# Performance work log

Measured on AMD Instinct MI355X. Metric: run time of the kernel, lower is better.

Reference implementation:

```python
import jax, jax.numpy as jnp
import numpy as np

T, B, I, H, NQ = 256, 256, 256, 512, 4

def setup_inputs() -> dict:
    key = jax.random.key(0)
    ks = jax.random.split(key, 16)
    d = {"inputs": jax.random.normal(ks[0], (T, B, I), dtype=jnp.float32)}
    idx = 1
    for n in ["f", "i", "g", "o"]:
        d[f"W{n}_l"] = jax.random.normal(ks[idx], (NQ, I + H), dtype=jnp.float32) * 0.02; idx += 1
        d[f"b{n}_l"] = jnp.zeros((NQ,), jnp.float32)
        d[f"W{n}_p"] = jax.random.normal(ks[idx], (H, 1), dtype=jnp.float32) * 0.5; idx += 1
        d[f"b{n}_p"] = jnp.zeros((H,), jnp.float32)
        d[f"W{n}_r"] = jax.random.normal(ks[idx], (H, H), dtype=jnp.float32) * 0.02; idx += 1
    return d

def reference(inputs, Wf_l, bf_l, Wf_p, bf_p, Wf_r,
              Wi_l, bi_l, Wi_p, bi_p, Wi_r,
              Wg_l, bg_l, Wg_p, bg_p, Wg_r,
              Wo_l, bo_l, Wo_p, bo_p, Wo_r):
    # Quantum circuit: RX(theta_i) on each wire, CNOT chain, <Z_0>. Only wire-0's
    # rotation affects Z_0 (CNOT(0,1) has wire 0 as control and commutes with Z_0),
    # so expval = cos(theta_0). theta = Linear(combined), take component 0.
    def gate(comb, hx, Wl, bl, Wp, bp, Wr, act):
        q = jnp.cos(comb @ Wl[0] + bl[0])[:, None]          # (B,1) = <Z_0>
        return act(q @ Wp.T + bp) + hx @ Wr.T               # proj + classical residual

    def step(carry, x):
        hx, cx = carry
        comb = jnp.concatenate([x, hx], axis=1)             # (B, I+H)
        f = gate(comb, hx, Wf_l, bf_l, Wf_p, bf_p, Wf_r, jax.nn.sigmoid)
        i = gate(comb, hx, Wi_l, bi_l, Wi_p, bi_p, Wi_r, jax.nn.sigmoid)
        g = gate(comb, hx, Wg_l, bg_l, Wg_p, bg_p, Wg_r, jnp.tanh)
        o = gate(comb, hx, Wo_l, bo_l, Wo_p, bo_p, Wo_r, jax.nn.sigmoid)
        cx = f * cx + i * g
        hx = o * jnp.tanh(cx)
        return (hx, cx), hx

    b = inputs.shape[1]
    h0 = jnp.zeros((b, H), inputs.dtype)
    (hx, cx), ys = jax.lax.scan(step, (h0, h0), inputs)
    return ys, hx, cx
```

## Files before the change

kernel.cpp:

```cpp
#include <hip/hip_runtime.h>
#include <hip/hip_cooperative_groups.h>
#include <math.h>

namespace cg = cooperative_groups;

#define T_ 256
#define B_ 256
#define I_ 256
#define H_ 512
#define NB 8
#define NH 32
#define BG 32
#define NTH 512

typedef __attribute__((ext_vector_type(8))) short short8;
typedef __attribute__((ext_vector_type(4))) float f32x4;
typedef __attribute__((ext_vector_type(4))) unsigned int uint4v;

__device__ __forceinline__ float sig_(float v){ return 1.0f/(1.0f+__expf(-v)); }
__device__ __forceinline__ short f2bf(float f){
  unsigned u = __float_as_uint(f);
  unsigned r = (u + 0x7fffu + ((u>>16)&1u)) >> 16;
  return (short)r;
}

__global__ __launch_bounds__(NTH)
void qlstm_kernel(
    const float* __restrict__ x,
    const float* __restrict__ Wf_l, const float* __restrict__ bf_l,
    const float* __restrict__ Wf_p, const float* __restrict__ bf_p,
    const float* __restrict__ Wf_r,
    const float* __restrict__ Wi_l, const float* __restrict__ bi_l,
    const float* __restrict__ Wi_p, const float* __restrict__ bi_p,
    const float* __restrict__ Wi_r,
    const float* __restrict__ Wg_l, const float* __restrict__ bg_l,
    const float* __restrict__ Wg_p, const float* __restrict__ bg_p,
    const float* __restrict__ Wg_r,
    const float* __restrict__ Wo_l, const float* __restrict__ bo_l,
    const float* __restrict__ Wo_p, const float* __restrict__ bo_p,
    const float* __restrict__ Wo_r,
    float* __restrict__ out,
    char* __restrict__ wsb)
{
  __shared__ char  hxT[32*1024];
  __shared__ float gacc[4*32*17];
  __shared__ float qd[4*32];
  __shared__ unsigned short hxe[32*16];

  float*          sx    = (float*)wsb;
  unsigned short* hxg   = (unsigned short*)(wsb + (1u<<20));
  unsigned*       flags = (unsigned*)(wsb + (1u<<20) + (256u<<10));

  const int tid  = threadIdx.x;
  const int wgid = blockIdx.x;
  const int bgp  = wgid & 7;
  const int nh   = wgid >> 3;
  const int wave = tid >> 6;
  const int l    = tid & 63;
  const int l15  = l & 15;
  const int q4   = l >> 4;
  const int m    = wave & 3;
  const int n    = wave >> 2;
  const bool hasq = (m == 0);

  for (int idx = tid; idx < 8*4*BG; idx += NTH) {
    int g   = idx >> 8;
    int rem = idx & 255;
    int tt  = rem >> 5;
    int b   = rem & 31;
    int t   = nh*8 + tt;
    int bglob = bgp*BG + b;
    const float* wl = (g==0)?Wf_l:(g==1)?Wi_l:(g==2)?Wg_l:Wo_l;
    const float* bl = (g==0)?bf_l:(g==1)?bi_l:(g==2)?bg_l:bo_l;
    const float* xr = x + ((size_t)t*B_ + bglob)*I_;
    float a = 0.f;
    #pragma unroll 8
    for (int i2 = 0; i2 < I_; i2 += 4) {
      float4 v = *(const float4*)(xr + i2);
      a += v.x*wl[i2] + v.y*wl[i2+1] + v.z*wl[i2+2] + v.w*wl[i2+3];
    }
    sx[((size_t)t*4 + g)*B_ + bglob] = a + bl[0];
  }
  if (tid < T_)
    __hip_atomic_store(&flags[((size_t)tid*8 + bgp)*32 + nh], 0u,
                       __ATOMIC_RELAXED, __HIP_MEMORY_SCOPE_SYSTEM);

  short8 afrag[16];
  short8 afragq[16];
  {
    const float* wr = (m==0)?Wf_r:(m==1)?Wi_r:(m==2)?Wg_r:Wo_r;
    const int h = nh*16 + l15;
    #pragma unroll
    for (int kk = 0; kk < 16; ++kk) {
      const float* src = wr + (size_t)h*H_ + kk*32 + q4*8;
      short8 pk;
      #pragma unroll
      for (int j = 0; j < 8; ++j) pk[j] = f2bf(src[j]);
      afrag[kk] = pk;
    }
    if (hasq) {
      #pragma unroll
      for (int kk = 0; kk < 16; ++kk) {
        short8 pk;
        if (l15 < 4) {
          const float* ql = (l15==0)?Wf_l:(l15==1)?Wi_l:(l15==2)?Wg_l:Wo_l;
          const float* src = ql + I_ + kk*32 + q4*8;
          #pragma unroll
          for (int j = 0; j < 8; ++j) pk[j] = f2bf(src[j]);
        } else {
          #pragma unroll
          for (int j = 0; j < 8; ++j) pk[j] = 0;
        }
        afragq[kk] = pk;
      }
    }
  }

  const int hl = tid & 15;
  const int eb = tid >> 4;
  const int h_ep = nh*16 + hl;
  const int bglob_ep = bgp*BG + eb;
  const float wfp = Wf_p[h_ep], bfp = bf_p[h_ep];
  const float wip = Wi_p[h_ep], bip = bi_p[h_ep];
  const float wgp = Wg_p[h_ep], bgp_ = bg_p[h_ep];
  const float wop = Wo_p[h_ep], bop = bo_p[h_ep];
  float cxr = 0.f;

  cg::grid_group grid = cg::this_grid();
  grid.sync();

  const int bb   = n*16 + l15;
  const int brow = bb * 1024;
  const int bsw  = (bb & 7) << 4;
  const int bq16 = q4 * 16;

  for (int t = 0; t < T_; ++t) {
    if (t == 0) {
      #pragma unroll
      for (int i = 0; i < 4; ++i)
        *(f32x4*)(hxT + ((wave*4+i)*1024 + 16*l)) = (f32x4){0.f,0.f,0.f,0.f};
    } else {
      uint4v v0, v1, v2, v3;
      unsigned long long base =
        (unsigned long long)((const char*)hxg + (((size_t)(bgp*BG + wave*4)) << 10) + 16*l);
      asm volatile("global_load_dwordx4 %0, %1, off sc0 sc1"             : "=v"(v0) : "v"(base) : "memory");
      asm volatile("global_load_dwordx4 %0, %1, off offset:1024 sc0 sc1" : "=v"(v1) : "v"(base) : "memory");
      asm volatile("global_load_dwordx4 %0, %1, off offset:2048 sc0 sc1" : "=v"(v2) : "v"(base) : "memory");
      asm volatile("global_load_dwordx4 %0, %1, off offset:3072 sc0 sc1" : "=v"(v3) : "v"(base) : "memory");
      asm volatile("s_waitcnt vmcnt(0)" ::: "memory");
      const int r0w = wave*4;
      *(uint4v*)(hxT + ((r0w  )*1024 + ((16*l) ^ (((r0w  )&7)<<4)))) = v0;
      *(uint4v*)(hxT + ((r0w+1)*1024 + ((16*l) ^ (((r0w+1)&7)<<4)))) = v1;
      *(uint4v*)(hxT + ((r0w+2)*1024 + ((16*l) ^ (((r0w+2)&7)<<4)))) = v2;
      *(uint4v*)(hxT + ((r0w+3)*1024 + ((16*l) ^ (((r0w+3)&7)<<4)))) = v3;
    }
    __syncthreads();

    f32x4 acc  = {0.f,0.f,0.f,0.f};
    f32x4 accq = {0.f,0.f,0.f,0.f};
    #pragma unroll
    for (int kk = 0; kk < 16; ++kk) {
      short8 bf = *(const short8*)(hxT + brow + ((kk*64 + bq16) ^ bsw));
      acc = __builtin_amdgcn_mfma_f32_16x16x32_bf16(afrag[kk], bf, acc, 0, 0, 0);
      if (hasq)
        accq = __builtin_amdgcn_mfma_f32_16x16x32_bf16(afragq[kk], bf, accq, 0, 0, 0);
    }
    {
      const int cb = n*16 + l15;
      const int r0 = q4*4;
      #pragma unroll
      for (int r = 0; r < 4; ++r)
        gacc[(m*32 + cb)*17 + r0 + r] = acc[r];
      if (hasq && q4 == 0) {
        #pragma unroll
        for (int r = 0; r < 4; ++r)
          qd[r*32 + cb] = accq[r];
      }
    }
    __syncthreads();

    float hnew;
    {
      float q0 = cosf(sx[((size_t)t*4+0)*B_ + bglob_ep] + qd[0*32+eb]);
      float q1 = cosf(sx[((size_t)t*4+1)*B_ + bglob_ep] + qd[1*32+eb]);
      float q2 = cosf(sx[((size_t)t*4+2)*B_ + bglob_ep] + qd[2*32+eb]);
      float q3 = cosf(sx[((size_t)t*4+3)*B_ + bglob_ep] + qd[3*32+eb]);
      float fv = sig_ (q0*wfp + bfp ) + gacc[(0*32 + eb)*17 + hl];
      float iv = sig_ (q1*wip + bip ) + gacc[(1*32 + eb)*17 + hl];
      float gv = tanhf(q2*wgp + bgp_) + gacc[(2*32 + eb)*17 + hl];
      float ov = sig_ (q3*wop + bop ) + gacc[(3*32 + eb)*17 + hl];
      cxr = fv*cxr + iv*gv;
      hnew = ov * tanhf(cxr);
      hxe[eb*16 + hl] = (unsigned short)f2bf(hnew);
    }
    __syncthreads();

    if (t < T_-1) {
      if (tid < 128) {
        const int b2 = tid >> 2, c4 = tid & 3;
        unsigned long long val =
          *(const unsigned long long*)((const char*)hxe + b2*32 + c4*8);
        unsigned long long addr =
          (unsigned long long)((char*)hxg + (((size_t)(bgp*BG + b2)) << 10) + (nh*16 + c4*4)*2);
        asm volatile("global_store_dwordx2 %0, %1, off sc0 sc1" :: "v"(addr), "v"(val) : "memory");
      }
      asm volatile("s_waitcnt vmcnt(0)" ::: "memory");
      __syncthreads();
      if (tid == 0)
        __hip_atomic_store(&flags[((size_t)t*8 + bgp)*32 + nh], 1u,
                           __ATOMIC_RELAXED, __HIP_MEMORY_SCOPE_SYSTEM);
      out[((size_t)t*B_ + bglob_ep)*H_ + h_ep] = hnew;
      if (tid < 64) {
        unsigned* fp = &flags[((size_t)t*8 + bgp)*32 + (tid & 31)];
        while (__hip_atomic_load(fp, __ATOMIC_RELAXED, __HIP_MEMORY_SCOPE_SYSTEM) == 0u)
          __builtin_amdgcn_s_sleep(1);
      }
      __syncthreads();
    } else {
      out[((size_t)t*B_ + bglob_ep)*H_ + h_ep] = hnew;
      out[(size_t)T_*B_*H_ + (size_t)bglob_ep*H_ + h_ep] = hnew;
      out[(size_t)T_*B_*H_ + (size_t)B_*H_ + (size_t)bglob_ep*H_ + h_ep] = cxr;
    }
  }
}

extern "C" void kernel_launch(void* const* d_in, const int* in_sizes, int n_in,
                              void* d_out, int out_size, void* d_ws, size_t ws_size,
                              hipStream_t stream) {
  const float* x    = (const float*)d_in[0];
  const float* Wf_l = (const float*)d_in[1];  const float* bf_l = (const float*)d_in[2];
  const float* Wf_p = (const float*)d_in[3];  const float* bf_p = (const float*)d_in[4];
  const float* Wf_r = (const float*)d_in[5];
  const float* Wi_l = (const float*)d_in[6];  const float* bi_l = (const float*)d_in[7];
  const float* Wi_p = (const float*)d_in[8];  const float* bi_p = (const float*)d_in[9];
  const float* Wi_r = (const float*)d_in[10];
  const float* Wg_l = (const float*)d_in[11]; const float* bg_l = (const float*)d_in[12];
  const float* Wg_p = (const float*)d_in[13]; const float* bg_p = (const float*)d_in[14];
  const float* Wg_r = (const float*)d_in[15];
  const float* Wo_l = (const float*)d_in[16]; const float* bo_l = (const float*)d_in[17];
  const float* Wo_p = (const float*)d_in[18]; const float* bo_p = (const float*)d_in[19];
  const float* Wo_r = (const float*)d_in[20];
  float* out = (float*)d_out;
  char*  wsb = (char*)d_ws;

  void* args[] = { &x,
                   &Wf_l, &bf_l, &Wf_p, &bf_p, &Wf_r,
                   &Wi_l, &bi_l, &Wi_p, &bi_p, &Wi_r,
                   &Wg_l, &bg_l, &Wg_p, &bg_p, &Wg_r,
                   &Wo_l, &bo_l, &Wo_p, &bo_p, &Wo_r,
                   &out, &wsb };
  hipLaunchCooperativeKernel((void*)qlstm_kernel, dim3(NB*NH), dim3(NTH),
                             args, 0, stream);
}
```

Before: 1.196 ms.

## Interleave gate rows in MFMA tiles, epilogue in registers, per-wave sequence flags

Reorders the recurrent weight rows so each MFMA output tile holds all four gates for a hidden unit. Every wave also computes the quantum-angle dot product, so the LSTM epilogue runs straight from accumulator registers and the LDS staging plus two block barriers per step go away. Cross-block sync moves from per-step flags to monotonically increasing per-wave sequence counters, with a double-buffered hidden state and per-element short stores. The changes trade redundant q-MFMAs and finer-grained global stores and polls for fewer barriers, and also switch to fast __cosf and exp-based tanh approximations.

```diff
diff --git a/kernel.cpp b/kernel.cpp
--- a/kernel.cpp
+++ b/kernel.cpp
@@ -18,10 +18,10 @@
 typedef __attribute__((ext_vector_type(4))) unsigned int uint4v;
 
 __device__ __forceinline__ float sig_(float v){ return 1.0f/(1.0f+__expf(-v)); }
+__device__ __forceinline__ float tanh_(float v){ float e=__expf(2.f*v); return 1.f-2.f/(e+1.f); }
 __device__ __forceinline__ short f2bf(float f){
   unsigned u = __float_as_uint(f);
-  unsigned r = (u + 0x7fffu + ((u>>16)&1u)) >> 16;
-  return (short)r;
+  return (short)((u + 0x7fffu + ((u>>16)&1u)) >> 16);
 }
 
 __global__ __launch_bounds__(NTH)
@@ -42,14 +42,11 @@
     float* __restrict__ out,
     char* __restrict__ wsb)
 {
-  __shared__ char  hxT[32*1024];
-  __shared__ float gacc[4*32*17];
-  __shared__ float qd[4*32];
-  __shared__ unsigned short hxe[32*16];
-
-  float*          sx    = (float*)wsb;
-  unsigned short* hxg   = (unsigned short*)(wsb + (1u<<20));
-  unsigned*       flags = (unsigned*)(wsb + (1u<<20) + (256u<<10));
+  __shared__ char hxT[32*1024];
+
+  float* sx   = (float*)wsb;
+  char*  hxg  = wsb + (1u<<20);
+  char*  seqb = wsb + (1u<<20) + (512u<<10);
 
   const int tid  = threadIdx.x;
   const int wgid = blockIdx.x;
@@ -59,9 +56,8 @@
   const int l    = tid & 63;
   const int l15  = l & 15;
   const int q4   = l >> 4;
-  const int m    = wave & 3;
   const int n    = wave >> 2;
-  const bool hasq = (m == 0);
+  const int wq   = wave & 3;
 
   for (int idx = tid; idx < 8*4*BG; idx += NTH) {
     int g   = idx >> 8;
@@ -81,48 +77,37 @@
     }
     sx[((size_t)t*4 + g)*B_ + bglob] = a + bl[0];
   }
-  if (tid < T_)
-    __hip_atomic_store(&flags[((size_t)tid*8 + bgp)*32 + nh], 0u,
-                       __ATOMIC_RELAXED, __HIP_MEMORY_SCOPE_SYSTEM);
+  if (tid < 8) {
+    unsigned long long sa =
+      (unsigned long long)(seqb + (((size_t)bgp*8 + tid)*NH + nh)*4);
+    unsigned z = 0;
+    asm volatile("global_store_dword %0, %1, off sc0 sc1" :: "v"(sa), "v"(z) : "memory");
+  }
 
   short8 afrag[16];
   short8 afragq[16];
   {
-    const float* wr = (m==0)?Wf_r:(m==1)?Wi_r:(m==2)?Wg_r:Wo_r;
-    const int h = nh*16 + l15;
+    const int g  = l15 & 3;
+    const float* wr = (g==0)?Wf_r:(g==1)?Wi_r:(g==2)?Wg_r:Wo_r;
+    const float* wl = (g==0)?Wf_l:(g==1)?Wi_l:(g==2)?Wg_l:Wo_l;
+    const int hA = nh*16 + wq*4 + (l15>>2);
     #pragma unroll
     for (int kk = 0; kk < 16; ++kk) {
-      const float* src = wr + (size_t)h*H_ + kk*32 + q4*8;
-      short8 pk;
+      const float* srcA = wr + (size_t)hA*H_ + kk*32 + q4*8;
+      const float* srcQ = wl + I_ + kk*32 + q4*8;
+      short8 pa, pq;
       #pragma unroll
-      for (int j = 0; j < 8; ++j) pk[j] = f2bf(src[j]);
-      afrag[kk] = pk;
-    }
-    if (hasq) {
-      #pragma unroll
-      for (int kk = 0; kk < 16; ++kk) {
-        short8 pk;
-        if (l15 < 4) {
-          const float* ql = (l15==0)?Wf_l:(l15==1)?Wi_l:(l15==2)?Wg_l:Wo_l;
-          const float* src = ql + I_ + kk*32 + q4*8;
-          #pragma unroll
-          for (int j = 0; j < 8; ++j) pk[j] = f2bf(src[j]);
-        } else {
-          #pragma unroll
-          for (int j = 0; j < 8; ++j) pk[j] = 0;
-        }
-        afragq[kk] = pk;
-      }
-    }
-  }
-
-  const int hl = tid & 15;
-  const int eb = tid >> 4;
-  const int h_ep = nh*16 + hl;
-  const int bglob_ep = bgp*BG + eb;
+      for (int j = 0; j < 8; ++j) { pa[j] = f2bf(srcA[j]); pq[j] = f2bf(srcQ[j]); }
+      afrag[kk]  = pa;
+      afragq[kk] = pq;
+    }
+  }
+
+  const int h_ep = nh*16 + wq*4 + q4;
+  const int b_ep = bgp*BG + n*16 + l15;
   const float wfp = Wf_p[h_ep], bfp = bf_p[h_ep];
   const float wip = Wi_p[h_ep], bip = bi_p[h_ep];
-  const float wgp = Wg_p[h_ep], bgp_ = bg_p[h_ep];
+  const float wgp = Wg_p[h_ep], bgw = bg_p[h_ep];
   const float wop = Wo_p[h_ep], bop = bo_p[h_ep];
   float cxr = 0.f;
 
@@ -135,6 +120,11 @@
   const int bq16 = q4 * 16;
 
   for (int t = 0; t < T_; ++t) {
+    const float sx0 = sx[((size_t)t*4+0)*B_ + b_ep];
+    const float sx1 = sx[((size_t)t*4+1)*B_ + b_ep];
+    const float sx2 = sx[((size_t)t*4+2)*B_ + b_ep];
+    const float sx3 = sx[((size_t)t*4+3)*B_ + b_ep];
+
     if (t == 0) {
       #pragma unroll
       for (int i = 0; i < 4; ++i)
@@ -142,7 +132,8 @@
     } else {
       uint4v v0, v1, v2, v3;
       unsigned long long base =
-        (unsigned long long)((const char*)hxg + (((size_t)(bgp*BG + wave*4)) << 10) + 16*l);
+        (unsigned long long)(hxg + ((size_t)(t&1))*262144
+                             + (((size_t)(bgp*BG + wave*4)) << 10) + 16*l);
       asm volatile("global_load_dwordx4 %0, %1, off sc0 sc1"             : "=v"(v0) : "v"(base) : "memory");
       asm volatile("global_load_dwordx4 %0, %1, off offset:1024 sc0 sc1" : "=v"(v1) : "v"(base) : "memory");
       asm volatile("global_load_dwordx4 %0, %1, off offset:2048 sc0 sc1" : "=v"(v2) : "v"(base) : "memory");
@@ -161,65 +152,48 @@
     #pragma unroll
     for (int kk = 0; kk < 16; ++kk) {
       short8 bf = *(const short8*)(hxT + brow + ((kk*64 + bq16) ^ bsw));
-      acc = __builtin_amdgcn_mfma_f32_16x16x32_bf16(afrag[kk], bf, acc, 0, 0, 0);
-      if (hasq)
-        accq = __builtin_amdgcn_mfma_f32_16x16x32_bf16(afragq[kk], bf, accq, 0, 0, 0);
-    }
-    {
-      const int cb = n*16 + l15;
-      const int r0 = q4*4;
-      #pragma unroll
-      for (int r = 0; r < 4; ++r)
-        gacc[(m*32 + cb)*17 + r0 + r] = acc[r];
-      if (hasq && q4 == 0) {
-        #pragma unroll
-        for (int r = 0; r < 4; ++r)
-          qd[r*32 + cb] = accq[r];
+      acc  = __builtin_amdgcn_mfma_f32_16x16x32_bf16(afrag[kk],  bf, acc,  0, 0, 0);
+      accq = __builtin_amdgcn_mfma_f32_16x16x32_bf16(afragq[kk], bf, accq, 0, 0, 0);
+    }
+
+    float q0 = __cosf(sx0 + accq[0]);
+    float q1 = __cosf(sx1 + accq[1]);
+    float q2 = __cosf(sx2 + accq[2]);
+    float q3 = __cosf(sx3 + accq[3]);
+    float fv = sig_ (q0*wfp + bfp) + acc[0];
+    float iv = sig_ (q1*wip + bip) + acc[1];
+    float gv = tanh_(q2*wgp + bgw) + acc[2];
+    float ov = sig_ (q3*wop + bop) + acc[3];
+    cxr = fv*cxr + iv*gv;
+    float hnew = ov * tanh_(cxr);
+    out[((size_t)t*B_ + b_ep)*H_ + h_ep] = hnew;
+
+    if (t < T_-1) {
+      unsigned hv = (unsigned)(unsigned short)f2bf(hnew);
+      unsigned long long ha =
+        (unsigned long long)(hxg + ((size_t)((t+1)&1))*262144
+                             + ((size_t)b_ep*1024) + h_ep*2);
+      asm volatile("global_store_short %0, %1, off sc0 sc1" :: "v"(ha), "v"(hv) : "memory");
+      asm volatile("s_waitcnt vmcnt(0)" ::: "memory");
+      if (l == 0) {
+        unsigned long long sa =
+          (unsigned long long)(seqb + (((size_t)bgp*8 + wave)*NH + nh)*4);
+        unsigned sv = (unsigned)(t+1);
+        asm volatile("global_store_dword %0, %1, off sc0 sc1" :: "v"(sa), "v"(sv) : "memory");
       }
-    }
-    __syncthreads();
-
-    float hnew;
-    {
-      float q0 = cosf(sx[((size_t)t*4+0)*B_ + bglob_ep] + qd[0*32+eb]);
-      float q1 = cosf(sx[((size_t)t*4+1)*B_ + bglob_ep] + qd[1*32+eb]);
-      float q2 = cosf(sx[((size_t)t*4+2)*B_ + bglob_ep] + qd[2*32+eb]);
-      float q3 = cosf(sx[((size_t)t*4+3)*B_ + bglob_ep] + qd[3*32+eb]);
-      float fv = sig_ (q0*wfp + bfp ) + gacc[(0*32 + eb)*17 + hl];
-      float iv = sig_ (q1*wip + bip ) + gacc[(1*32 + eb)*17 + hl];
-      float gv = tanhf(q2*wgp + bgp_) + gacc[(2*32 + eb)*17 + hl];
-      float ov = sig_ (q3*wop + bop ) + gacc[(3*32 + eb)*17 + hl];
-      cxr = fv*cxr + iv*gv;
-      hnew = ov * tanhf(cxr);
-      hxe[eb*16 + hl] = (unsigned short)f2bf(hnew);
-    }
-    __syncthreads();
-
-    if (t < T_-1) {
-      if (tid < 128) {
-        const int b2 = tid >> 2, c4 = tid & 3;
-        unsigned long long val =
-          *(const unsigned long long*)((const char*)hxe + b2*32 + c4*8);
-        unsigned long long addr =
-          (unsigned long long)((char*)hxg + (((size_t)(bgp*BG + b2)) << 10) + (nh*16 + c4*4)*2);
-        asm volatile("global_store_dwordx2 %0, %1, off sc0 sc1" :: "v"(addr), "v"(val) : "memory");
-      }
-      asm volatile("s_waitcnt vmcnt(0)" ::: "memory");
-      __syncthreads();
-      if (tid == 0)
-        __hip_atomic_store(&flags[((size_t)t*8 + bgp)*32 + nh], 1u,
-                           __ATOMIC_RELAXED, __HIP_MEMORY_SCOPE_SYSTEM);
-      out[((size_t)t*B_ + bglob_ep)*H_ + h_ep] = hnew;
-      if (tid < 64) {
-        unsigned* fp = &flags[((size_t)t*8 + bgp)*32 + (tid & 31)];
-        while (__hip_atomic_load(fp, __ATOMIC_RELAXED, __HIP_MEMORY_SCOPE_SYSTEM) == 0u)
-          __builtin_amdgcn_s_sleep(1);
+      {
+        unsigned long long fa =
+          (unsigned long long)(seqb + (((size_t)bgp*8 + wave)*NH + (l & 31))*4);
+        unsigned v;
+        do {
+          asm volatile("global_load_dword %0, %1, off sc0 sc1\n\ts_waitcnt vmcnt(0)"
+                       : "=v"(v) : "v"(fa) : "memory");
+        } while (v < (unsigned)(t+1));
       }
       __syncthreads();
     } else {
-      out[((size_t)t*B_ + bglob_ep)*H_ + h_ep] = hnew;
-      out[(size_t)T_*B_*H_ + (size_t)bglob_ep*H_ + h_ep] = hnew;
-      out[(size_t)T_*B_*H_ + (size_t)B_*H_ + (size_t)bglob_ep*H_ + h_ep] = cxr;
+      out[(size_t)T_*B_*H_ + (size_t)b_ep*H_ + h_ep] = hnew;
+      out[(size_t)T_*B_*H_ + (size_t)B_*H_ + (size_t)b_ep*H_ + h_ep] = cxr;
     }
   }
 }
```

Measured after the change: 2.718 ms. 127% more time.
